# Optimization experiments

Hardware: AMD Instinct MI355X
Metric: run time of the kernel (lower is better)

Reference implementation:

```python
import jax, jax.numpy as jnp
import numpy as np
import math

PHI = (1.0 + math.sqrt(5.0)) / 2.0
B, S, E, H = 4, 1024, 1024, 16
D = E // H  # head_dim = 64


def setup_inputs() -> dict:
    key = jax.random.key(0)
    ks = jax.random.split(key, 16)
    w = 0.02  # stand-in for xavier(gain=1/phi); math is init-agnostic
    inp = {
        "query": jax.random.normal(ks[0], (B, S, E), jnp.float32),
        "key": jax.random.normal(ks[1], (B, S, E), jnp.float32),
        "value": jax.random.normal(ks[2], (B, S, E), jnp.float32),
        "consciousness_levels": jax.random.uniform(ks[3], (B, S), jnp.float32),
        # causal mask, broadcast over batch and heads
        "attn_mask": jnp.tril(jnp.ones((S, S), bool))[None, None],
        # projection weights stored [in, out] (torch Linear applies x @ W.T)
        "Wq": jax.random.normal(ks[4], (E, E), jnp.float32) * w,
        "bq": jnp.zeros((E,), jnp.float32),
        "Wk": jax.random.normal(ks[5], (E, E), jnp.float32) * w,
        "bk": jnp.zeros((E,), jnp.float32),
        "Wv": jax.random.normal(ks[6], (E, E), jnp.float32) * w,
        "bv": jnp.zeros((E,), jnp.float32),
        "Wo": jax.random.normal(ks[7], (E, E), jnp.float32) * w,
        "bo": jnp.zeros((E,), jnp.float32),
        "Wc": jax.random.normal(ks[8], (E, H), jnp.float32) * w,
        "bc": jnp.zeros((H,), jnp.float32),
        # phi_bias[h] = (h+1)/phi**(h+1), shape [H,1,1] as in _init_weights
        "phi_bias": jnp.array([(h + 1) / PHI ** (h + 1) for h in range(H)],
                               jnp.float32).reshape(H, 1, 1),
    }
    return inp


def reference(query, key, value, consciousness_levels, attn_mask,
              Wq, bq, Wk, bk, Wv, bv, Wo, bo, Wc, bc, phi_bias):
    # project and split heads: [B,S,E] -> [B,H,S,D]
    q = (query @ Wq + bq).reshape(B, S, H, D).transpose(0, 2, 1, 3)
    k = (key @ Wk + bk).reshape(B, S, H, D).transpose(0, 2, 1, 3)
    v = (value @ Wv + bv).reshape(B, S, H, D).transpose(0, 2, 1, 3)

    inv_scale = 1.0 / (math.sqrt(D) * math.sqrt(PHI))  # phi-scaled 1/sqrt(d)
    scores = jnp.einsum('bhqd,bhkd->bhqk', q, k) * inv_scale
    scores = scores + phi_bias[None]                   # per-head additive bias
    scores = jnp.where(attn_mask, scores, -jnp.inf)
    attn = jax.nn.softmax(scores, axis=-1)             # [B,H,S,S]

    # consciousness reweighting + second softmax (faithful to original)
    cw = jax.nn.softmax(query @ Wc + bc, axis=-1)      # [B,S,H]
    cw = cw.transpose(0, 2, 1)[..., None]              # [B,H,S,1]
    cb = consciousness_levels[:, None, :, None]        # [B,1,S,1]
    attn = jax.nn.softmax(attn * (1.0 + cb * cw), axis=-1)

    ctx = jnp.einsum('bhqk,bhkd->bhqd', attn, v)
    ctx = ctx.transpose(0, 2, 1, 3).reshape(B, S, E)
    out = ctx @ Wo + bo
    return out, attn
```

## Files before the change

kernel.cpp:

```cpp
#include <hip/hip_runtime.h>
#include <stdint.h>

#define B_ 4
#define S_ 1024
#define E_ 1024
#define H_ 16
#define D_ 64

typedef unsigned short u16;
typedef short s16x8 __attribute__((ext_vector_type(8)));
typedef unsigned short u16x8 __attribute__((ext_vector_type(8)));
typedef unsigned short u16x4 __attribute__((ext_vector_type(4)));
typedef unsigned short u16x2 __attribute__((ext_vector_type(2)));
typedef float f32x4 __attribute__((ext_vector_type(4)));

__device__ __forceinline__ u16 f2bf(float f) {
    union { float f; uint32_t i; } x; x.f = f;
    uint32_t r = (x.i + 0x7FFFu + ((x.i >> 16) & 1u)) >> 16;
    return (u16)r;
}

__device__ __forceinline__ float wave_sum(float v) {
    #pragma unroll
    for (int o = 32; o; o >>= 1) v += __shfl_xor(v, o);
    return v;
}

__device__ __forceinline__ void gload16(const u16* g, u16* l) {
    __builtin_amdgcn_global_load_lds(
        (const __attribute__((address_space(1))) void*)g,
        (__attribute__((address_space(3))) void*)l, 16, 0, 0);
}

template<int BM, int BN>
__device__ __forceinline__ void gemm_core(
    const u16* __restrict__ Ab, int lda,
    const u16* __restrict__ Bp, int ldb,
    int m0, int n0, int K,
    u16* As, u16* Bs, f32x4 (&acc)[BM / 32][BN / 32])
{
    constexpr int FM = BM / 32, FN = BN / 32;
    constexpr int ACH = BM / 64;
    constexpr int BCH = BN / 64;
    const int t = threadIdx.x, lane = t & 63, w = t >> 6;
    const int wr = w >> 1, wc = w & 1, al = lane & 15, aq = lane >> 4;

    auto stage = [&](int buf, int k0) {
        u16* Ad = As + buf * (BM * 32);
        u16* Bd = Bs + buf * (BN * 32);
        #pragma unroll
        for (int i = 0; i < ACH; i++) {
            const int c = i * 256 + w * 64 + lane;
            gload16(Ab + (size_t)(m0 + (c >> 2)) * lda + k0 + (c & 3) * 8,
                    Ad + (size_t)(i * 256 + w * 64) * 8);
        }
        #pragma unroll
        for (int i = 0; i < BCH; i++) {
            const int c = i * 256 + w * 64 + lane;
            gload16(Bp + (size_t)(n0 + (c >> 2)) * ldb + k0 + (c & 3) * 8,
                    Bd + (size_t)(i * 256 + w * 64) * 8);
        }
    };
    auto compute = [&](int buf) {
        const u16* Ar = As + buf * (BM * 32);
        const u16* Br = Bs + buf * (BN * 32);
        s16x8 af[FM], bf[FN];
        #pragma unroll
        for (int i = 0; i < FM; i++)
            af[i] = *(const s16x8*)(Ar + ((wr * FM + i) * 16 + al) * 32 + aq * 8);
        #pragma unroll
        for (int j = 0; j < FN; j++)
            bf[j] = *(const s16x8*)(Br + ((wc * FN + j) * 16 + al) * 32 + aq * 8);
        #pragma unroll
        for (int i = 0; i < FM; i++)
            #pragma unroll
            for (int j = 0; j < FN; j++)
                acc[i][j] = __builtin_amdgcn_mfma_f32_16x16x32_bf16(af[i], bf[j], acc[i][j], 0, 0, 0);
    };

    int cur = 0;
    stage(0, 0);
    for (int k0 = 32; k0 < K; k0 += 32) {
        asm volatile("s_waitcnt vmcnt(0)" ::: "memory");
        __syncthreads();
        stage(cur ^ 1, k0);
        compute(cur);
        cur ^= 1;
    }
    asm volatile("s_waitcnt vmcnt(0)" ::: "memory");
    __syncthreads();
    compute(cur);
}

__global__ __launch_bounds__(256, 3)
void gemm_qkv(const u16* __restrict__ qbf, const u16* __restrict__ kbf,
              const u16* __restrict__ vbf, const u16* __restrict__ wt,
              const float* __restrict__ bq, const float* __restrict__ bk,
              const float* __restrict__ bv,
              u16* __restrict__ q_ws, u16* __restrict__ k_ws,
              u16* __restrict__ vt_ws)
{
    __shared__ __attribute__((aligned(16))) u16 As[2 * 128 * 32];
    __shared__ __attribute__((aligned(16))) u16 Bs[2 * 128 * 32];
    const int flat = blockIdx.x + (blockIdx.y << 3) + (blockIdx.z << 8);
    const int z = flat >> 8;
    const int y = flat & 31;
    const int x = (flat >> 5) & 7;
    const u16* Ab = (z == 0) ? qbf : (z == 1) ? kbf : vbf;
    const u16* Bp = wt + (size_t)z * E_ * E_;
    const float* bias = (z == 0) ? bq : (z == 1) ? bk : bv;
    u16* Cb = (z == 0) ? q_ws : (z == 1) ? k_ws : vt_ws;
    const int m0 = y * 128, n0 = x * 128;

    f32x4 acc[4][4];
    #pragma unroll
    for (int i = 0; i < 4; i++)
        #pragma unroll
        for (int j = 0; j < 4; j++)
            acc[i][j] = (f32x4){0.f, 0.f, 0.f, 0.f};

    gemm_core<128, 128>(Ab, E_, Bp, E_, m0, n0, E_, As, Bs, acc);

    const int t = threadIdx.x, lane = t & 63, w = t >> 6;
    const int wr = w >> 1, wc = w & 1, al = lane & 15, aq = lane >> 4;
    #pragma unroll
    for (int i = 0; i < 4; i++) {
        #pragma unroll
        for (int j = 0; j < 4; j++) {
            const int col = n0 + (wc * 4 + j) * 16 + al;
            const float bvv = bias[col];
            #pragma unroll
            for (int r = 0; r < 4; r++) {
                const int row = m0 + (wr * 4 + i) * 16 + aq * 4 + r;
                const float vv = acc[i][j][r] + bvv;
                const int b = row >> 10, s = row & 1023, h = col >> 6, d = col & 63;
                if (z < 2)
                    Cb[((size_t)((b * H_ + h) * S_ + s)) * D_ + d] = f2bf(vv);
                else
                    Cb[((size_t)((b * H_ + h) * D_ + d)) * S_ + s] = f2bf(vv);
            }
        }
    }
}

__global__ __launch_bounds__(256, 3)
void gemm_o(const u16* __restrict__ ctx, const u16* __restrict__ wt3,
            const float* __restrict__ bo, float* __restrict__ out)
{
    __shared__ __attribute__((aligned(16))) u16 As[2 * 128 * 32];
    __shared__ __attribute__((aligned(16))) u16 Bs[2 * 64 * 32];
    const int flat = blockIdx.x + (blockIdx.y << 4);
    const int y = flat & 31;
    const int x = flat >> 5;
    const int m0 = y * 128, n0 = x * 64;

    f32x4 acc[4][2];
    #pragma unroll
    for (int i = 0; i < 4; i++)
        #pragma unroll
        for (int j = 0; j < 2; j++)
            acc[i][j] = (f32x4){0.f, 0.f, 0.f, 0.f};

    gemm_core<128, 64>(ctx, E_, wt3, E_, m0, n0, E_, As, Bs, acc);

    const int t = threadIdx.x, lane = t & 63, w = t >> 6;
    const int wr = w >> 1, wc = w & 1, al = lane & 15, aq = lane >> 4;
    #pragma unroll
    for (int i = 0; i < 4; i++) {
        #pragma unroll
        for (int j = 0; j < 2; j++) {
            const int col = n0 + (wc * 2 + j) * 16 + al;
            const float bvv = bo[col];
            #pragma unroll
            for (int r = 0; r < 4; r++) {
                const int row = m0 + (wr * 4 + i) * 16 + aq * 4 + r;
                __builtin_nontemporal_store(acc[i][j][r] + bvv,
                                            &out[(size_t)row * E_ + col]);
            }
        }
    }
}

__global__ __launch_bounds__(256)
void prelude_k(const float* __restrict__ query, const float* __restrict__ key_,
               const float* __restrict__ value,
               const float* __restrict__ Wq, const float* __restrict__ Wk,
               const float* __restrict__ Wv, const float* __restrict__ Wo,
               const float* __restrict__ Wc, const float* __restrict__ bc,
               const float* __restrict__ cl,
               u16* __restrict__ qbf, u16* __restrict__ kbf,
               u16* __restrict__ vbf, u16* __restrict__ wt,
               float* __restrict__ mws)
{
    __shared__ float tile[64][65];
    const int bid = blockIdx.x, t = threadIdx.x;

    if (bid < 512) {
        const int tid = bid * 256 + t;
        #pragma unroll
        for (int j = 0; j < 4; j++) {
            const int i = tid + j * 131072;
            {
                f32x4 a = *(const f32x4*)(query + (size_t)i * 8);
                f32x4 b = *(const f32x4*)(query + (size_t)i * 8 + 4);
                u16x8 o;
                o[0] = f2bf(a[0]); o[1] = f2bf(a[1]); o[2] = f2bf(a[2]); o[3] = f2bf(a[3]);
                o[4] = f2bf(b[0]); o[5] = f2bf(b[1]); o[6] = f2bf(b[2]); o[7] = f2bf(b[3]);
                *(u16x8*)(qbf + (size_t)i * 8) = o;
            }
            {
                f32x4 a = *(const f32x4*)(key_ + (size_t)i * 8);
                f32x4 b = *(const f32x4*)(key_ + (size_t)i * 8 + 4);
                u16x8 o;
                o[0] = f2bf(a[0]); o[1] = f2bf(a[1]); o[2] = f2bf(a[2]); o[3] = f2bf(a[3]);
                o[4] = f2bf(b[0]); o[5] = f2bf(b[1]); o[6] = f2bf(b[2]); o[7] = f2bf(b[3]);
                *(u16x8*)(kbf + (size_t)i * 8) = o;
            }
            {
                f32x4 a = *(const f32x4*)(value + (size_t)i * 8);
                f32x4 b = *(const f32x4*)(value + (size_t)i * 8 + 4);
                u16x8 o;
                o[0] = f2bf(a[0]); o[1] = f2bf(a[1]); o[2] = f2bf(a[2]); o[3] = f2bf(a[3]);
                o[4] = f2bf(b[0]); o[5] = f2bf(b[1]); o[6] = f2bf(b[2]); o[7] = f2bf(b[3]);
                *(u16x8*)(vbf + (size_t)i * 8) = o;
            }
        }
    } else if (bid < 1536) {
        const int tb = bid - 512;
        const int zz = tb >> 8, rem = tb & 255;
        const int by = (rem >> 4) * 64, bx = (rem & 15) * 64;
        const float* in = (zz == 0) ? Wq : (zz == 1) ? Wk : (zz == 2) ? Wv : Wo;
        u16* o = wt + (size_t)zz * E_ * E_;
        const int tx = t & 63, ty = t >> 6;
        #pragma unroll
        for (int i = 0; i < 16; i++) {
            const int r = ty + i * 4;
            tile[r][tx] = in[(size_t)(by + r) * E_ + bx + tx];
        }
        __syncthreads();
        #pragma unroll
        for (int i = 0; i < 16; i++) {
            const int r = ty + i * 4;
            o[(size_t)(bx + r) * E_ + by + tx] = f2bf(tile[tx][r]);
        }
    } else {
        const int lane = t & 63, wave = t >> 6;
        const int r = (bid - 1536) * 4 + wave;
        const float* qrow = query + (size_t)r * E_;
        float acc[H_];
        #pragma unroll
        for (int c = 0; c < H_; c++) acc[c] = 0.f;
        for (int e = lane; e < E_; e += 64) {
            float qv = qrow[e];
            const float* wp = Wc + e * H_;
            f32x4 w0 = *(const f32x4*)(wp);
            f32x4 w1 = *(const f32x4*)(wp + 4);
            f32x4 w2 = *(const f32x4*)(wp + 8);
            f32x4 w3 = *(const f32x4*)(wp + 12);
            #pragma unroll
            for (int c = 0; c < 4; c++) {
                acc[c]      += qv * w0[c];
                acc[4 + c]  += qv * w1[c];
                acc[8 + c]  += qv * w2[c];
                acc[12 + c] += qv * w3[c];
            }
        }
        #pragma unroll
        for (int c = 0; c < H_; c++) acc[c] = wave_sum(acc[c]);
        float mx = -3e38f;
        #pragma unroll
        for (int c = 0; c < H_; c++) { acc[c] += bc[c]; mx = fmaxf(mx, acc[c]); }
        float se = 0.f;
        #pragma unroll
        for (int c = 0; c < H_; c++) { acc[c] = __expf(acc[c] - mx); se += acc[c]; }
        if (lane < H_) {
            float mycw = 0.f;
            #pragma unroll
            for (int c = 0; c < H_; c++) if (lane == c) mycw = acc[c];
            mycw /= se;
            int b = r >> 10, s = r & 1023;
            float clv = cl[r];
            mws[((size_t)(b * H_ + lane)) * S_ + s] = 1.f + clv * mycw;
        }
    }
}

#define LDP 1048
__global__ __launch_bounds__(512, 4)
void attn_fused(const u16* __restrict__ q_ws, const u16* __restrict__ k_ws,
                const u16* __restrict__ vt_ws, const float* __restrict__ mws,
                float* __restrict__ attn_out, u16* __restrict__ ctx_ws,
                float alpha)
{
    __shared__ __attribute__((aligned(16))) char shraw[8 * 64 * 20 * 4];
    u16*   Pl  = (u16*)shraw;
    float* dmp = (float*)shraw;
    __shared__ float red[8 * 16];
    __shared__ float sclA[16], invzA[16];

    const int t = threadIdx.x, lane = t & 63, w = t >> 6;
    const int al = lane & 15, aq = lane >> 4;
    const int bh = blockIdx.x;
    const int q0 = blockIdx.y << 4;

    const u16* Qp = q_ws + ((size_t)bh * S_ + q0) * D_;
    const u16* Kp = k_ws + ((size_t)bh * S_ + w * 128) * D_;
    const u16* Vp = vt_ws + (size_t)bh * D_ * S_;

    s16x8 qa0 = *(const s16x8*)(Qp + (size_t)al * D_ + aq * 8);
    s16x8 qa1 = *(const s16x8*)(Qp + (size_t)al * D_ + 32 + aq * 8);
    f32x4 ee[8];
    f32x4 s1 = (f32x4){0.f, 0.f, 0.f, 0.f};
    #pragma unroll
    for (int mf = 0; mf < 8; mf++) {
        const u16* kr = Kp + (size_t)(mf * 16 + al) * D_ + aq * 8;
        s16x8 kb0 = *(const s16x8*)(kr);
        s16x8 kb1 = *(const s16x8*)(kr + 32);
        f32x4 a0 = (f32x4){0.f, 0.f, 0.f, 0.f};
        a0 = __builtin_amdgcn_mfma_f32_16x16x32_bf16(qa0, kb0, a0, 0, 0, 0);
        a0 = __builtin_amdgcn_mfma_f32_16x16x32_bf16(qa1, kb1, a0, 0, 0, 0);
        const int kk = w * 128 + mf * 16 + al;
        #pragma unroll
        for (int r = 0; r < 4; r++) {
            const int qg = q0 + aq * 4 + r;
            float e = (kk <= qg) ? __expf(a0[r] * alpha) : 0.f;
            ee[mf][r] = e;
            s1[r] += e;
        }
    }
    #pragma unroll
    for (int o = 1; o <= 8; o <<= 1) {
        #pragma unroll
        for (int r = 0; r < 4; r++) s1[r] += __shfl_xor(s1[r], o);
    }
    if (al == 0) {
        #pragma unroll
        for (int r = 0; r < 4; r++) red[w * 16 + aq * 4 + r] = s1[r];
    }
    __syncthreads();
    if (t < 16) {
        float s = 0.f;
        #pragma unroll
        for (int c = 0; c < 8; c++) s += red[c * 16 + t];
        sclA[t] = mws[(size_t)bh * S_ + q0 + t] / s;
    }
    __syncthreads();

    float scl_r[4];
    #pragma unroll
    for (int r = 0; r < 4; r++) scl_r[r] = sclA[aq * 4 + r];
    f32x4 s2 = (f32x4){0.f, 0.f, 0.f, 0.f};
    #pragma unroll
    for (int mf = 0; mf < 8; mf++) {
        const int kk = w * 128 + mf * 16 + al;
        #pragma unroll
        for (int r = 0; r < 4; r++) {
            const int qg = q0 + aq * 4 + r;
            float e = (kk <= qg) ? __expf(ee[mf][r] * scl_r[r]) : 1.f;
            ee[mf][r] = e;
            s2[r] += e;
        }
    }
    #pragma unroll
    for (int o = 1; o <= 8; o <<= 1) {
        #pragma unroll
        for (int r = 0; r < 4; r++) s2[r] += __shfl_xor(s2[r], o);
    }
    if (al == 0) {
        #pragma unroll
        for (int r = 0; r < 4; r++) red[w * 16 + aq * 4 + r] = s2[r];
    }
    __syncthreads();
    if (t < 16) {
        float s = 0.f;
        #pragma unroll
        for (int c = 0; c < 8; c++) s += red[c * 16 + t];
        invzA[t] = 1.f / s;
    }
    __syncthreads();

    float iz_r[4];
    #pragma unroll
    for (int r = 0; r < 4; r++) iz_r[r] = invzA[aq * 4 + r];
    float* ao = attn_out + (size_t)bh * S_ * S_ + (size_t)q0 * S_;
    #pragma unroll
    for (int mf = 0; mf < 8; mf++) {
        const int kk = w * 128 + mf * 16 + al;
        #pragma unroll
        for (int r = 0; r < 4; r++) {
            const int rq = aq * 4 + r;
            __builtin_nontemporal_store(ee[mf][r] * iz_r[r],
                                        &ao[(size_t)rq * S_ + kk]);
            Pl[(size_t)rq * LDP + kk] = f2bf(ee[mf][r]);
        }
    }
    __syncthreads();

    f32x4 pa[4];
    #pragma unroll
    for (int nf = 0; nf < 4; nf++) pa[nf] = (f32x4){0.f, 0.f, 0.f, 0.f};
    #pragma unroll
    for (int ks = 0; ks < 4; ks++) {
        const int kb = w * 128 + ks * 32;
        s16x8 af = *(const s16x8*)(Pl + (size_t)al * LDP + kb + aq * 8);
        #pragma unroll
        for (int nf = 0; nf < 4; nf++) {
            s16x8 bv = *(const s16x8*)(Vp + (size_t)(nf * 16 + al) * S_ + kb + aq * 8);
            pa[nf] = __builtin_amdgcn_mfma_f32_16x16x32_bf16(af, bv, pa[nf], 0, 0, 0);
        }
    }
    __syncthreads();

    {
        float* dp = dmp + w * (64 * 20);
        #pragma unroll
        for (int nf = 0; nf < 4; nf++)
            *(f32x4*)(dp + (size_t)(nf * 16 + al) * 20 + aq * 4) = pa[nf];
    }
    __syncthreads();
    {
        const int r5 = t >> 5, d0 = (t & 31) * 2;
        const float iz = invzA[r5];
        float o0 = 0.f, o1 = 0.f;
        #pragma unroll
        for (int ww = 0; ww < 8; ww++) {
            const float* rp5 = dmp + ww * (64 * 20) + r5;
            o0 += rp5[(size_t)d0 * 20];
            o1 += rp5[(size_t)(d0 + 1) * 20];
        }
        const int b = bh >> 4, h = bh & 15;
        u16* cp = ctx_ws + ((size_t)(b * S_ + q0 + r5)) * E_ + h * 64 + d0;
        u16x2 ob;
        ob[0] = f2bf(o0 * iz);
        ob[1] = f2bf(o1 * iz);
        *(u16x2*)cp = ob;
    }
}

extern "C" void kernel_launch(void* const* d_in, const int* in_sizes, int n_in,
                              void* d_out, int out_size, void* d_ws, size_t ws_size,
                              hipStream_t stream)
{
    const float* query = (const float*)d_in[0];
    const float* key_  = (const float*)d_in[1];
    const float* value = (const float*)d_in[2];
    const float* cl    = (const float*)d_in[3];
    const float* Wq = (const float*)d_in[5];
    const float* bq = (const float*)d_in[6];
    const float* Wk = (const float*)d_in[7];
    const float* bk = (const float*)d_in[8];
    const float* Wv = (const float*)d_in[9];
    const float* bv = (const float*)d_in[10];
    const float* Wo = (const float*)d_in[11];
    const float* bo = (const float*)d_in[12];
    const float* Wc = (const float*)d_in[13];
    const float* bc = (const float*)d_in[14];

    float* out  = (float*)d_out;
    float* attn = out + (size_t)B_ * S_ * E_;

    u16* q_ws   = (u16*)d_ws;
    u16* k_ws   = q_ws  + (size_t)B_ * S_ * E_;
    u16* vt_ws  = k_ws  + (size_t)B_ * S_ * E_;
    u16* ctx_ws = vt_ws + (size_t)B_ * S_ * E_;
    u16* wt     = ctx_ws + (size_t)B_ * S_ * E_;
    float* mws  = (float*)(wt + (size_t)4 * E_ * E_);

    u16* qbf = (u16*)attn;
    u16* kbf = qbf + (size_t)B_ * S_ * E_;
    u16* vbf = kbf + (size_t)B_ * S_ * E_;

    const float inv_scale = 0.09826892502579689f;
    dim3 blk(256);

    prelude_k<<<2560, blk, 0, stream>>>(query, key_, value, Wq, Wk, Wv, Wo,
                                        Wc, bc, cl, qbf, kbf, vbf, wt, mws);

    gemm_qkv<<<dim3(8, 32, 3), blk, 0, stream>>>(
        qbf, kbf, vbf, wt, bq, bk, bv, q_ws, k_ws, vt_ws);

    attn_fused<<<dim3(B_ * H_, S_ / 16), dim3(512), 0, stream>>>(
        q_ws, k_ws, vt_ws, mws, attn, ctx_ws, inv_scale);

    gemm_o<<<dim3(16, 32, 1), blk, 0, stream>>>(
        ctx_ws, wt + (size_t)3 * E_ * E_, bo, out);
}
```

Measured before the change: 526.5 us.

## Stage transposed score tile in LDS for coalesced vectorized attention stores

The QK^T MFMA operands are swapped so each lane holds four consecutive key columns of one query row. The fp32 probability tile is staged in shared memory, and the attention matrix is then written back as row-contiguous float4 nontemporal stores instead of scattered scalar stores. The bf16 conversion for the PV MFMA now happens on reads from the fp32 LDS tile. This trades a larger shared-memory footprint (about 64KB), which may cut occupancy, for coalesced global writes of the large attn output and simpler row reductions.

```diff
diff --git a/kernel.cpp b/kernel.cpp
--- a/kernel.cpp
+++ b/kernel.cpp
@@ -285,16 +285,15 @@
     }
 }
 
-#define LDP 1048
+#define LDS_ 1028
 __global__ __launch_bounds__(512, 4)
 void attn_fused(const u16* __restrict__ q_ws, const u16* __restrict__ k_ws,
                 const u16* __restrict__ vt_ws, const float* __restrict__ mws,
                 float* __restrict__ attn_out, u16* __restrict__ ctx_ws,
                 float alpha)
 {
-    __shared__ __attribute__((aligned(16))) char shraw[8 * 64 * 20 * 4];
-    u16*   Pl  = (u16*)shraw;
-    float* dmp = (float*)shraw;
+    __shared__ __attribute__((aligned(16))) float Sf[16 * LDS_];
+    float* dmp = Sf;
     __shared__ float red[8 * 16];
     __shared__ float sclA[16], invzA[16];
 
@@ -307,36 +306,30 @@
     const u16* Kp = k_ws + ((size_t)bh * S_ + w * 128) * D_;
     const u16* Vp = vt_ws + (size_t)bh * D_ * S_;
 
-    s16x8 qa0 = *(const s16x8*)(Qp + (size_t)al * D_ + aq * 8);
-    s16x8 qa1 = *(const s16x8*)(Qp + (size_t)al * D_ + 32 + aq * 8);
+    s16x8 qb0 = *(const s16x8*)(Qp + (size_t)al * D_ + aq * 8);
+    s16x8 qb1 = *(const s16x8*)(Qp + (size_t)al * D_ + 32 + aq * 8);
+    const int qg = q0 + al;
     f32x4 ee[8];
-    f32x4 s1 = (f32x4){0.f, 0.f, 0.f, 0.f};
+    float s1 = 0.f;
     #pragma unroll
     for (int mf = 0; mf < 8; mf++) {
         const u16* kr = Kp + (size_t)(mf * 16 + al) * D_ + aq * 8;
-        s16x8 kb0 = *(const s16x8*)(kr);
-        s16x8 kb1 = *(const s16x8*)(kr + 32);
+        s16x8 ka0 = *(const s16x8*)(kr);
+        s16x8 ka1 = *(const s16x8*)(kr + 32);
         f32x4 a0 = (f32x4){0.f, 0.f, 0.f, 0.f};
-        a0 = __builtin_amdgcn_mfma_f32_16x16x32_bf16(qa0, kb0, a0, 0, 0, 0);
-        a0 = __builtin_amdgcn_mfma_f32_16x16x32_bf16(qa1, kb1, a0, 0, 0, 0);
-        const int kk = w * 128 + mf * 16 + al;
+        a0 = __builtin_amdgcn_mfma_f32_16x16x32_bf16(ka0, qb0, a0, 0, 0, 0);
+        a0 = __builtin_amdgcn_mfma_f32_16x16x32_bf16(ka1, qb1, a0, 0, 0, 0);
+        const int k0i = w * 128 + mf * 16 + aq * 4;
         #pragma unroll
         for (int r = 0; r < 4; r++) {
-            const int qg = q0 + aq * 4 + r;
-            float e = (kk <= qg) ? __expf(a0[r] * alpha) : 0.f;
+            float e = (k0i + r <= qg) ? __expf(a0[r] * alpha) : 0.f;
             ee[mf][r] = e;
-            s1[r] += e;
-        }
-    }
-    #pragma unroll
-    for (int o = 1; o <= 8; o <<= 1) {
-        #pragma unroll
-        for (int r = 0; r < 4; r++) s1[r] += __shfl_xor(s1[r], o);
-    }
-    if (al == 0) {
-        #pragma unroll
-        for (int r = 0; r < 4; r++) red[w * 16 + aq * 4 + r] = s1[r];
-    }
+            s1 += e;
+        }
+    }
+    s1 += __shfl_xor(s1, 16);
+    s1 += __shfl_xor(s1, 32);
+    if (lane < 16) red[w * 16 + al] = s1;
     __syncthreads();
     if (t < 16) {
         float s = 0.f;
@@ -346,30 +339,21 @@
     }
     __syncthreads();
 
-    float scl_r[4];
-    #pragma unroll
-    for (int r = 0; r < 4; r++) scl_r[r] = sclA[aq * 4 + r];
-    f32x4 s2 = (f32x4){0.f, 0.f, 0.f, 0.f};
+    const float sl = sclA[al];
+    float s2 = 0.f;
     #pragma unroll
     for (int mf = 0; mf < 8; mf++) {
-        const int kk = w * 128 + mf * 16 + al;
+        const int k0i = w * 128 + mf * 16 + aq * 4;
         #pragma unroll
         for (int r = 0; r < 4; r++) {
-            const int qg = q0 + aq * 4 + r;
-            float e = (kk <= qg) ? __expf(ee[mf][r] * scl_r[r]) : 1.f;
+            float e = (k0i + r <= qg) ? __expf(ee[mf][r] * sl) : 1.f;
             ee[mf][r] = e;
-            s2[r] += e;
-        }
-    }
-    #pragma unroll
-    for (int o = 1; o <= 8; o <<= 1) {
-        #pragma unroll
-        for (int r = 0; r < 4; r++) s2[r] += __shfl_xor(s2[r], o);
-    }
-    if (al == 0) {
-        #pragma unroll
-        for (int r = 0; r < 4; r++) red[w * 16 + aq * 4 + r] = s2[r];
-    }
+            s2 += e;
+        }
+    }
+    s2 += __shfl_xor(s2, 16);
+    s2 += __shfl_xor(s2, 32);
+    if (lane < 16) red[w * 16 + al] = s2;
     __syncthreads();
     if (t < 16) {
         float s = 0.f;
@@ -377,24 +361,27 @@
         for (int c = 0; c < 8; c++) s += red[c * 16 + t];
         invzA[t] = 1.f / s;
     }
-    __syncthreads();
-
-    float iz_r[4];
-    #pragma unroll
-    for (int r = 0; r < 4; r++) iz_r[r] = invzA[aq * 4 + r];
+    #pragma unroll
+    for (int mf = 0; mf < 8; mf++) {
+        const int k0i = w * 128 + mf * 16 + aq * 4;
+        *(f32x4*)(Sf + (size_t)al * LDS_ + k0i) = ee[mf];
+    }
+    __syncthreads();
+
     float* ao = attn_out + (size_t)bh * S_ * S_ + (size_t)q0 * S_;
     #pragma unroll
-    for (int mf = 0; mf < 8; mf++) {
-        const int kk = w * 128 + mf * 16 + al;
-        #pragma unroll
-        for (int r = 0; r < 4; r++) {
-            const int rq = aq * 4 + r;
-            __builtin_nontemporal_store(ee[mf][r] * iz_r[r],
-                                        &ao[(size_t)rq * S_ + kk]);
-            Pl[(size_t)rq * LDP + kk] = f2bf(ee[mf][r]);
-        }
-    }
-    __syncthreads();
+    for (int rr = 0; rr < 2; rr++) {
+        const int r2 = w * 2 + rr;
+        const float iz = invzA[r2];
+        #pragma unroll
+        for (int k2 = 0; k2 < 4; k2++) {
+            f32x4 v = *(const f32x4*)(Sf + (size_t)r2 * LDS_ + k2 * 256 + lane * 4);
+            f32x4 o;
+            #pragma unroll
+            for (int j = 0; j < 4; j++) o[j] = v[j] * iz;
+            __builtin_nontemporal_store(o, (f32x4*)(ao + (size_t)r2 * S_ + k2 * 256 + lane * 4));
+        }
+    }
 
     f32x4 pa[4];
     #pragma unroll
@@ -402,7 +389,14 @@
     #pragma unroll
     for (int ks = 0; ks < 4; ks++) {
         const int kb = w * 128 + ks * 32;
-        s16x8 af = *(const s16x8*)(Pl + (size_t)al * LDP + kb + aq * 8);
+        const float* ap = Sf + (size_t)al * LDS_ + kb + aq * 8;
+        f32x4 x0 = *(const f32x4*)(ap);
+        f32x4 x1 = *(const f32x4*)(ap + 4);
+        s16x8 af;
+        af[0] = (short)f2bf(x0[0]); af[1] = (short)f2bf(x0[1]);
+        af[2] = (short)f2bf(x0[2]); af[3] = (short)f2bf(x0[3]);
+        af[4] = (short)f2bf(x1[0]); af[5] = (short)f2bf(x1[1]);
+        af[6] = (short)f2bf(x1[2]); af[7] = (short)f2bf(x1[3]);
         #pragma unroll
         for (int nf = 0; nf < 4; nf++) {
             s16x8 bv = *(const s16x8*)(Vp + (size_t)(nf * 16 + al) * S_ + kb + aq * 8);
```

Result: no change. 535.9 us (+1.8%).
